# Kernel optimization log

Measured on AMD Instinct MI355X. Metric: run time of the kernel, lower is better.

The kernel has to match this reference:

```python
import jax, jax.numpy as jnp
import numpy as np
from jax import lax

H, W, K, MAXN = 93, 44, 2, 24          # face grid, hop count, (2K+1)^2-1 neighbors
HID, LAT, OUT, B = 128, 1024, 2, 8


def _neighbor_lookup():
    """Static k-hop box neighbor indices/counts for each grid position."""
    HW = H * W
    idx = np.zeros((HW, MAXN), np.int32)
    cnt = np.zeros((HW,), np.int32)
    for r in range(H):
        for c in range(W):
            p = r * W + c
            n = []
            for dr in range(-K, K + 1):
                for dc in range(-K, K + 1):
                    if dr == 0 and dc == 0:
                        continue
                    rr, cc = r + dr, c + dc
                    if 0 <= rr < H and 0 <= cc < W:
                        n.append(rr * W + cc)
            cnt[p] = len(n)
            idx[p, :len(n)] = n
    return jnp.asarray(idx), jnp.asarray(cnt)


def _gelu(x):
    return jax.nn.gelu(x, approximate=False)  # torch default GELU is exact erf


def _group_norm(x, gamma, beta, groups=8, eps=1e-5):
    b, c, h, w = x.shape
    xg = x.reshape(b, groups, c // groups, h, w)
    mu = xg.mean(axis=(2, 3, 4), keepdims=True)
    var = xg.var(axis=(2, 3, 4), keepdims=True)
    xg = (xg - mu) * lax.rsqrt(var + eps)
    return xg.reshape(b, c, h, w) * gamma[None, :, None, None] + beta[None, :, None, None]


def setup_inputs() -> dict:
    key = jax.random.key(0)
    ks = jax.random.split(key, 10)
    s = 0.05
    nbr_idx, nbr_cnt = _neighbor_lookup()
    return {
        "face_tensor": jax.random.normal(ks[0], (B, 2, H, W), jnp.float32),
        "latent_token": jax.random.normal(ks[1], (B, LAT), jnp.float32),
        "mask_2d": jax.random.randint(ks[2], (B, H, W), 0, 2, jnp.int32),
        "nbr_indices": nbr_idx,
        "nbr_counts": nbr_cnt,
        # latent_proj
        "Wl": jax.random.normal(ks[3], (LAT, HID), jnp.float32) * s,
        "bl": jnp.zeros((HID,), jnp.float32),
        # global_decoder: ConvTranspose2d(3x3,pad1) -> GN(8) -> GELU -> Conv2d(3x3,pad1) -> GELU
        "Wt": jax.random.normal(ks[4], (3, 3, HID, HID), jnp.float32) * s,
        "bt": jnp.zeros((HID,), jnp.float32),
        "g1": jnp.ones((HID,), jnp.float32),
        "b1g": jnp.zeros((HID,), jnp.float32),
        "Wc": jax.random.normal(ks[5], (3, 3, HID, HID), jnp.float32) * s,
        "bc": jnp.zeros((HID,), jnp.float32),
        # attention scorer
        "Wa": jax.random.normal(ks[6], (HID,), jnp.float32) * s,
        "ba": jnp.zeros((), jnp.float32),
        # masked_pred_head MLP
        "W1": jax.random.normal(ks[7], (2 * HID, HID), jnp.float32) * s,
        "b1": jnp.zeros((HID,), jnp.float32),
        "W2": jax.random.normal(ks[8], (HID, OUT), jnp.float32) * s,
        "b2": jnp.zeros((OUT,), jnp.float32),
    }


def reference(face_tensor, latent_token, mask_2d, nbr_indices, nbr_counts,
              Wl, bl, Wt, bt, g1, b1g, Wc, bc, Wa, ba, W1, b1, W2, b2):
    Bn, C, Hh, Ww = face_tensor.shape
    HW = Hh * Ww
    dn = ("NCHW", "HWIO", "NCHW")

    # --- feature extraction (global decoder branch) ---
    latent_cond = _gelu(latent_token @ Wl + bl)                      # (B, HID)
    x = jnp.broadcast_to(latent_cond[:, :, None, None], (Bn, HID, Hh, Ww))
    f = lax.conv_transpose(x, Wt, (1, 1), "SAME", dimension_numbers=dn) + bt[None, :, None, None]
    f = _gelu(_group_norm(f, g1, b1g))
    f = lax.conv_general_dilated(f, Wc, (1, 1), "SAME", dimension_numbers=dn) + bc[None, :, None, None]
    f = _gelu(f)
    feats = f.reshape(Bn, HID, HW).transpose(0, 2, 1)                # (B, HW, HID)

    # --- masked-neighbor attention pooling (computed for every position, padded layout) ---
    mask_flat = mask_2d.reshape(Bn, HW)
    in_range = jnp.arange(MAXN)[None, :] < nbr_counts[:, None]        # (HW, 24)
    nbr_masked = jnp.take(mask_flat, nbr_indices, axis=1)             # (B, HW, 24)
    valid = in_range[None] & (nbr_masked == 0)
    nbr_feat = jnp.take(feats, nbr_indices, axis=1)                   # (B, HW, 24, HID)
    logits = jnp.einsum("bpnh,h->bpn", nbr_feat, Wa) + ba
    logits = jnp.where(valid, logits, jnp.float32(-10000.0))
    attn = jax.nn.softmax(logits, axis=-1)
    attended = jnp.einsum("bpn,bpnh->bph", attn, nbr_feat)            # (B, HW, HID)

    combined = jnp.concatenate(
        [attended, jnp.broadcast_to(latent_cond[:, None, :], (Bn, HW, HID))], axis=-1)
    preds = _gelu(combined @ W1 + b1) @ W2 + b2                       # (B, HW, OUT)

    # --- pack masked positions to front of each row (fixed capacity HW instead of dynamic max_masked) ---
    m = mask_flat > 0
    within = jnp.cumsum(m, axis=1) - 1                                # slot for each masked position
    tgt = jnp.where(m, within, HW)                                    # unmasked go to dump slot HW
    brow = jnp.arange(Bn)[:, None]
    pred_packed = jnp.zeros((Bn, HW + 1, OUT), preds.dtype).at[brow, tgt].set(preds)[:, :HW]
    pos = jnp.arange(HW)
    rc = jnp.stack([pos // Ww, pos % Ww], axis=-1).astype(jnp.int32)  # (HW, 2)
    mask_indices = jnp.zeros((Bn, HW + 1, 2), jnp.int32).at[brow, tgt].set(
        jnp.broadcast_to(rc[None], (Bn, HW, 2)))[:, :HW]
    valid_mask = jnp.zeros((Bn, HW + 1), bool).at[brow, tgt].set(m)[:, :HW]
    return pred_packed, mask_indices, valid_mask
```

## Files before the change

### kernel.cpp

```cpp
#include <hip/hip_runtime.h>
#include <cmath>

#define HH   93
#define WWID 44
#define HWSZ 4092
#define NMAX 24
#define HID  128
#define LATD 1024
#define NB   8

__device__ __forceinline__ float gelu_f(float x) {
  return 0.5f * x * (1.0f + erff(x * 0.70710678118654752440f));
}

__device__ __constant__ int c_map[5][3] = {{-1,0,1},{0,1,1},{1,1,1},{1,1,2},{1,2,-1}};

__global__ __launch_bounds__(1024) void k_tap10(
    const float* __restrict__ latent, const float* __restrict__ Wl,
    const float* __restrict__ bl,
    const float* __restrict__ Wt, const float* __restrict__ W1, const float* __restrict__ b1p,
    float* __restrict__ u, float* __restrict__ cbo, float* __restrict__ outz)
{
  const int tap = blockIdx.x, b = blockIdx.y, tid = threadIdx.x;
  const int h4 = tid & 31, ig = tid >> 5;
  __shared__ float red[32 * HID];
  __shared__ float lc_s[HID];

  {
    const int gtid = (b * 10 + tap) * 1024 + tid;
    float4* oz = (float4*)outz;
    if (gtid < (NB*HWSZ*5)/4) oz[gtid] = make_float4(0.f, 0.f, 0.f, 0.f);
  }

  {
    const float* lat = latent + b * LATD;
    const float4* w4 = (const float4*)Wl;
    float4 a = make_float4(0.f, 0.f, 0.f, 0.f);
    for (int i0 = 0; i0 < 32; i0 += 8) {
      float  lv[8];
      float4 wv[8];
      #pragma unroll
      for (int j = 0; j < 8; ++j) {
        const int L = ig*32 + i0 + j;
        lv[j] = lat[L];
        wv[j] = w4[L*32 + h4];
      }
      #pragma unroll
      for (int j = 0; j < 8; ++j) {
        a.x = fmaf(lv[j], wv[j].x, a.x);
        a.y = fmaf(lv[j], wv[j].y, a.y);
        a.z = fmaf(lv[j], wv[j].z, a.z);
        a.w = fmaf(lv[j], wv[j].w, a.w);
      }
    }
    ((float4*)red)[ig*32 + h4] = a;
  }
  __syncthreads();
  if (tid < HID) {
    float s = bl[tid];
    #pragma unroll 8
    for (int g = 0; g < 32; ++g) s += red[g*HID + tid];
    lc_s[tid] = gelu_f(s);
  }
  __syncthreads();

  const float4* wt4 = (tap < 9) ? ((const float4*)(Wt + tap*HID*HID))
                                : ((const float4*)(W1 + HID*HID));
  float4 aa = make_float4(0.f, 0.f, 0.f, 0.f);
  #pragma unroll
  for (int j = 0; j < 4; ++j) {
    const int I = ig*4 + j;
    const float lv = lc_s[I];
    const float4 wv = wt4[I*32 + h4];
    aa.x = fmaf(lv, wv.x, aa.x); aa.y = fmaf(lv, wv.y, aa.y);
    aa.z = fmaf(lv, wv.z, aa.z); aa.w = fmaf(lv, wv.w, aa.w);
  }
  __syncthreads();
  ((float4*)red)[ig*32 + h4] = aa;
  __syncthreads();
  if (tid < HID) {
    float s = 0.f;
    #pragma unroll 8
    for (int g = 0; g < 32; ++g) s += red[g*HID + tid];
    if (tap < 9) u[(b*10 + tap)*HID + tid] = s;
    else         cbo[b*HID + tid] = b1p[tid] + s;
  }
}

__global__ __launch_bounds__(256) void k_case(
    const float* __restrict__ u, const float* __restrict__ bt,
    const float* __restrict__ g1p, const float* __restrict__ b1g,
    const float* __restrict__ Wc, const float* __restrict__ bc,
    const float* __restrict__ Wa, const float* __restrict__ ba,
    const float* __restrict__ W1,
    float* __restrict__ logito, float* __restrict__ projo)
{
  const int cs = blockIdx.x, b = blockIdx.y;
  const int r5 = cs / 5, c5 = cs % 5;
  const int tid = threadIdx.x, o4 = tid & 31, ig = tid >> 5;
  __shared__ float f2s[9 * HID];
  __shared__ float red[8 * HID];
  __shared__ float f3s[HID];
  __shared__ float red2[2];

  if (tid < HID) {
    const int t = tid;
    float uv[9];
    #pragma unroll
    for (int k = 0; k < 9; ++k) uv[k] = u[(b*10 + k)*HID + t];
    float ur[3][3];
    #pragma unroll
    for (int kc = 0; kc < 3; ++kc) {
      ur[0][kc] = uv[3+kc] + uv[6+kc];
      ur[1][kc] = uv[0+kc] + uv[3+kc] + uv[6+kc];
      ur[2][kc] = uv[0+kc] + uv[3+kc];
    }
    const float btv = bt[t];
    float f1v[9];
    #pragma unroll
    for (int a = 0; a < 3; ++a) {
      f1v[a*3+0] = btv + ur[a][1] + ur[a][2];
      f1v[a*3+1] = btv + ur[a][0] + ur[a][1] + ur[a][2];
      f1v[a*3+2] = btv + ur[a][0] + ur[a][1];
    }
    const float wr[3] = {1.f, (float)(HH-2), 1.f};
    const float wc[3] = {1.f, (float)(WWID-2), 1.f};
    float s1 = 0.f, s2 = 0.f;
    #pragma unroll
    for (int a = 0; a < 3; ++a)
      #pragma unroll
      for (int c = 0; c < 3; ++c) {
        const float w = wr[a] * wc[c];
        const float v = f1v[a*3+c];
        s1 += w * v;
        s2 += w * v * v;
      }
    #pragma unroll
    for (int off = 1; off < 16; off <<= 1) {
      s1 += __shfl_xor(s1, off);
      s2 += __shfl_xor(s2, off);
    }
    const float invN = 1.f / (float)(16 * HWSZ);
    const float mean = s1 * invN;
    const float var  = s2 * invN - mean * mean;
    const float sc = rsqrtf(var + 1e-5f) * g1p[t];
    const float sh = b1g[t] - mean * sc;
    #pragma unroll
    for (int k = 0; k < 9; ++k)
      f2s[k*HID + t] = gelu_f(fmaf(f1v[k], sc, sh));
  }
  __syncthreads();

  float4 a = make_float4(0.f, 0.f, 0.f, 0.f);
  #pragma unroll
  for (int kr = 0; kr < 3; ++kr) {
    const int rm = c_map[r5][kr];
    if (rm < 0) continue;
    #pragma unroll
    for (int kc = 0; kc < 3; ++kc) {
      const int cm = c_map[c5][kc];
      if (cm < 0) continue;
      const float4* w4 = (const float4*)(Wc + (kr*3 + kc)*HID*HID);
      const float* f2p = &f2s[(rm*3 + cm)*HID];
      #pragma unroll
      for (int i = 0; i < 16; ++i) {
        const int I = ig*16 + i;
        const float f = f2p[I];
        const float4 wv = w4[I*32 + o4];
        a.x = fmaf(f, wv.x, a.x); a.y = fmaf(f, wv.y, a.y);
        a.z = fmaf(f, wv.z, a.z); a.w = fmaf(f, wv.w, a.w);
      }
    }
  }
  ((float4*)red)[ig*32 + o4] = a;
  __syncthreads();

  if (tid < HID) {
    float s = bc[tid];
    #pragma unroll
    for (int g = 0; g < 8; ++g) s += red[g*HID + tid];
    const float f3v = gelu_f(s);
    f3s[tid] = f3v;
    float pl = f3v * Wa[tid];
    #pragma unroll
    for (int off = 1; off < 64; off <<= 1) pl += __shfl_xor(pl, off);
    if ((tid & 63) == 0) red2[tid >> 6] = pl;
  }
  __syncthreads();

  const float4* w14 = (const float4*)W1;
  float4 aa = make_float4(0.f, 0.f, 0.f, 0.f);
  #pragma unroll
  for (int i = 0; i < 16; ++i) {
    const int I = ig*16 + i;
    const float f = f3s[I];
    const float4 wv = w14[I*32 + o4];
    aa.x = fmaf(f, wv.x, aa.x); aa.y = fmaf(f, wv.y, aa.y);
    aa.z = fmaf(f, wv.z, aa.z); aa.w = fmaf(f, wv.w, aa.w);
  }
  __syncthreads();
  ((float4*)red)[ig*32 + o4] = aa;
  __syncthreads();
  if (tid < HID) {
    float s = 0.f;
    #pragma unroll
    for (int g = 0; g < 8; ++g) s += red[g*HID + tid];
    projo[(b*25 + cs)*HID + tid] = s;
  }
  if (tid == 0) logito[b*32 + cs] = red2[0] + red2[1] + ba[0];
}

__global__ __launch_bounds__(256) void k_pospack(
    const int* __restrict__ mask, const int* __restrict__ nbr_idx, const int* __restrict__ nbr_cnt,
    const float* __restrict__ logiti,
    const float* __restrict__ proji, const float* __restrict__ cbasei,
    const float* __restrict__ W2, const float* __restrict__ b2,
    float* __restrict__ out)
{
  const int b = blockIdx.y, chunk = blockIdx.x, tid = threadIdx.x;
  __shared__ float4 proj_s[25 * 32];
  __shared__ float4 cbase_s[32];
  __shared__ float  logit_s[32];
  __shared__ float  w2_s[2 * HID];
  __shared__ float  ippart[2][2];
  __shared__ int    bcnt_s[4];
  __shared__ int    wcnt_s[4];

  const float4* pj = (const float4*)(proji + b*25*HID);
  for (int i = tid; i < 25*32; i += 256) proj_s[i] = pj[i];
  if (tid < 32) cbase_s[tid] = ((const float4*)(cbasei + b*HID))[tid];
  if (tid < 32) logit_s[tid] = (tid < 25) ? logiti[b*32 + tid] : 0.f;
  w2_s[tid] = W2[tid];

  const int p0 = chunk * 128;
  {
    int cnt = 0;
    const int4* m4 = (const int4*)(mask + b*HWSZ);
    for (int i = tid; i < (p0 >> 2); i += 256) {
      const int4 v = m4[i];
      cnt += (v.x > 0) + (v.y > 0) + (v.z > 0) + (v.w > 0);
    }
    #pragma unroll
    for (int off = 1; off < 64; off <<= 1) cnt += __shfl_xor(cnt, off);
    if ((tid & 63) == 0) bcnt_s[tid >> 6] = cnt;
  }
  __syncthreads();

  if (tid < HID) {
    const float g = gelu_f(((const float*)proj_s)[12*HID + tid] + ((const float*)cbase_s)[tid]);
    float q0 = g * w2_s[tid*2 + 0];
    float q1 = g * w2_s[tid*2 + 1];
    #pragma unroll
    for (int off = 1; off < 64; off <<= 1) {
      q0 += __shfl_xor(q0, off);
      q1 += __shfl_xor(q1, off);
    }
    if ((tid & 63) == 0) { ippart[tid >> 6][0] = q0; ippart[tid >> 6][1] = q1; }
  }
  __syncthreads();
  const int   base = bcnt_s[0] + bcnt_s[1] + bcnt_s[2] + bcnt_s[3];
  const float ip0 = ippart[0][0] + ippart[1][0] + b2[0];
  const float ip1 = ippart[0][1] + ippart[1][1] + b2[1];

  const int p = p0 + (tid >> 1);
  const int half = tid & 1;
  const bool pok = (p < HWSZ);
  const int pc = pok ? p : 0;
  const int r = pc / WWID, cc = pc % WWID;
  const bool interior = (r >= 4) && (r <= HH-5) && (cc >= 4) && (cc <= WWID-5);
  const bool mp = pok && (mask[b*HWSZ + pc] > 0);

  float pr0 = ip0, pr1 = ip1;
  if (pok && !interior) {
    const int cnt = nbr_cnt[pc];
    float ev[NMAX];
    int   cid[NMAX];
    #pragma unroll
    for (int n = 0; n < NMAX; ++n) {
      const int q = nbr_idx[pc*NMAX + n];
      const int qr = q / WWID, qc = q % WWID;
      const int r5 = (qr == 0) ? 0 : (qr == 1) ? 1 : (qr == HH-2) ? 3 : (qr == HH-1) ? 4 : 2;
      const int c5 = (qc == 0) ? 0 : (qc == 1) ? 1 : (qc == WWID-2) ? 3 : (qc == WWID-1) ? 4 : 2;
      const int cd = r5*5 + c5;
      cid[n] = cd;
      const bool ok = (n < cnt) && (mask[b*HWSZ + q] == 0);
      ev[n] = ok ? logit_s[cd] : -10000.0f;
    }
    float mx = ev[0];
    #pragma unroll
    for (int n = 1; n < NMAX; ++n) mx = fmaxf(mx, ev[n]);
    float s = 0.f;
    #pragma unroll
    for (int n = 0; n < NMAX; ++n) { ev[n] = expf(ev[n] - mx); s += ev[n]; }
    const float inv = 1.f / s;

    float a0 = 0.f, a1 = 0.f;
    const int hb = half * 16;
    #pragma unroll 4
    for (int hq = 0; hq < 16; ++hq) {
      float4 a = make_float4(0.f, 0.f, 0.f, 0.f);
      #pragma unroll
      for (int n = 0; n < NMAX; ++n) {
        const float4 pv = proj_s[cid[n]*32 + hb + hq];
        const float w = ev[n];
        a.x = fmaf(w, pv.x, a.x);
        a.y = fmaf(w, pv.y, a.y);
        a.z = fmaf(w, pv.z, a.z);
        a.w = fmaf(w, pv.w, a.w);
      }
      const float4 cb = cbase_s[hb + hq];
      const int h0 = (hb + hq) * 4;
      const float g0 = gelu_f(fmaf(inv, a.x, cb.x));
      const float g1v = gelu_f(fmaf(inv, a.y, cb.y));
      const float g2 = gelu_f(fmaf(inv, a.z, cb.z));
      const float g3 = gelu_f(fmaf(inv, a.w, cb.w));
      a0 = fmaf(g0, w2_s[(h0+0)*2+0], a0); a1 = fmaf(g0, w2_s[(h0+0)*2+1], a1);
      a0 = fmaf(g1v, w2_s[(h0+1)*2+0], a0); a1 = fmaf(g1v, w2_s[(h0+1)*2+1], a1);
      a0 = fmaf(g2, w2_s[(h0+2)*2+0], a0); a1 = fmaf(g2, w2_s[(h0+2)*2+1], a1);
      a0 = fmaf(g3, w2_s[(h0+3)*2+0], a0); a1 = fmaf(g3, w2_s[(h0+3)*2+1], a1);
    }
    a0 += __shfl_xor(a0, 1);
    a1 += __shfl_xor(a1, 1);
    pr0 = a0 + b2[0];
    pr1 = a1 + b2[1];
  }

  const unsigned long long bal = __ballot(mp && half == 0);
  const int lane = tid & 63;
  const int myidx = __popcll(bal & ((1ull << lane) - 1ull));
  if (lane == 0) wcnt_s[tid >> 6] = (int)__popcll(bal);
  __syncthreads();
  int wbase = 0;
  for (int w = 0; w < (tid >> 6); ++w) wbase += wcnt_s[w];
  if (mp && half == 0) {
    const int slot = base + wbase + myidx;
    float* predo = out + b*HWSZ*2;
    float* idxo  = out + NB*HWSZ*2 + b*HWSZ*2;
    float* valo  = out + NB*HWSZ*4 + b*HWSZ;
    predo[slot*2 + 0] = pr0;
    predo[slot*2 + 1] = pr1;
    idxo[slot*2 + 0] = (float)r;
    idxo[slot*2 + 1] = (float)cc;
    valo[slot] = 1.0f;
  }
}

extern "C" void kernel_launch(void* const* d_in, const int* in_sizes, int n_in,
                              void* d_out, int out_size, void* d_ws, size_t ws_size,
                              hipStream_t stream) {
  (void)in_sizes; (void)n_in; (void)out_size; (void)ws_size;
  const float* latent  = (const float*)d_in[1];
  const int*   mask    = (const int*)d_in[2];
  const int*   nbr_idx = (const int*)d_in[3];
  const int*   nbr_cnt = (const int*)d_in[4];
  const float* Wl  = (const float*)d_in[5];
  const float* bl  = (const float*)d_in[6];
  const float* Wt  = (const float*)d_in[7];
  const float* bt  = (const float*)d_in[8];
  const float* g1p = (const float*)d_in[9];
  const float* b1g = (const float*)d_in[10];
  const float* Wc  = (const float*)d_in[11];
  const float* bc  = (const float*)d_in[12];
  const float* Wa  = (const float*)d_in[13];
  const float* ba  = (const float*)d_in[14];
  const float* W1  = (const float*)d_in[15];
  const float* b1p = (const float*)d_in[16];
  const float* W2  = (const float*)d_in[17];
  const float* b2  = (const float*)d_in[18];

  float* ws    = (float*)d_ws;
  float* u     = ws;
  float* logit = ws + 10240;
  float* proj  = ws + 10496;
  float* cbase = ws + 36096;

  dim3 gA(10, NB);
  k_tap10<<<gA, 1024, 0, stream>>>(latent, Wl, bl, Wt, W1, b1p, u, cbase, (float*)d_out);
  dim3 gB(25, NB);
  k_case<<<gB, 256, 0, stream>>>(u, bt, g1p, b1g, Wc, bc, Wa, ba, W1, logit, proj);
  dim3 gC(32, NB);
  k_pospack<<<gC, 256, 0, stream>>>(mask, nbr_idx, nbr_cnt, logit, proj, cbase, W2, b2,
                                    (float*)d_out);
}
```

Before: 47.07 us.

## Precompute per-chunk mask prefix counts in extra k_case block; pad proj_s rows

```diff
diff --git a/kernel.cpp b/kernel.cpp
--- a/kernel.cpp
+++ b/kernel.cpp
@@ -92,12 +92,34 @@
     const float* __restrict__ g1p, const float* __restrict__ b1g,
     const float* __restrict__ Wc, const float* __restrict__ bc,
     const float* __restrict__ Wa, const float* __restrict__ ba,
-    const float* __restrict__ W1,
-    float* __restrict__ logito, float* __restrict__ projo)
+    const float* __restrict__ W1, const int* __restrict__ mask,
+    float* __restrict__ logito, float* __restrict__ projo, int* __restrict__ chunkbase)
 {
   const int cs = blockIdx.x, b = blockIdx.y;
+  const int tid = threadIdx.x;
+
+  if (cs == 25) {
+    if (tid < 32) {
+      const int4* m4 = (const int4*)(mask + b*HWSZ);
+      const int n4 = (tid == 31) ? 31 : 32;
+      int cnt = 0;
+      for (int i = 0; i < n4; ++i) {
+        const int4 v = m4[tid*32 + i];
+        cnt += (v.x > 0) + (v.y > 0) + (v.z > 0) + (v.w > 0);
+      }
+      int s = cnt;
+      #pragma unroll
+      for (int off = 1; off < 32; off <<= 1) {
+        const int t = __shfl_up(s, off);
+        if (tid >= off) s += t;
+      }
+      chunkbase[b*32 + tid] = s - cnt;
+    }
+    return;
+  }
+
   const int r5 = cs / 5, c5 = cs % 5;
-  const int tid = threadIdx.x, o4 = tid & 31, ig = tid >> 5;
+  const int o4 = tid & 31, ig = tid >> 5;
   __shared__ float f2s[9 * HID];
   __shared__ float red[8 * HID];
   __shared__ float f3s[HID];
@@ -215,39 +237,26 @@
     const float* __restrict__ logiti,
     const float* __restrict__ proji, const float* __restrict__ cbasei,
     const float* __restrict__ W2, const float* __restrict__ b2,
+    const int* __restrict__ chunkbase,
     float* __restrict__ out)
 {
   const int b = blockIdx.y, chunk = blockIdx.x, tid = threadIdx.x;
-  __shared__ float4 proj_s[25 * 32];
+  __shared__ float4 proj_s[25 * 33];
   __shared__ float4 cbase_s[32];
   __shared__ float  logit_s[32];
   __shared__ float  w2_s[2 * HID];
   __shared__ float  ippart[2][2];
-  __shared__ int    bcnt_s[4];
   __shared__ int    wcnt_s[4];
 
   const float4* pj = (const float4*)(proji + b*25*HID);
-  for (int i = tid; i < 25*32; i += 256) proj_s[i] = pj[i];
+  for (int i = tid; i < 25*32; i += 256) proj_s[(i >> 5)*33 + (i & 31)] = pj[i];
   if (tid < 32) cbase_s[tid] = ((const float4*)(cbasei + b*HID))[tid];
   if (tid < 32) logit_s[tid] = (tid < 25) ? logiti[b*32 + tid] : 0.f;
   w2_s[tid] = W2[tid];
-
-  const int p0 = chunk * 128;
-  {
-    int cnt = 0;
-    const int4* m4 = (const int4*)(mask + b*HWSZ);
-    for (int i = tid; i < (p0 >> 2); i += 256) {
-      const int4 v = m4[i];
-      cnt += (v.x > 0) + (v.y > 0) + (v.z > 0) + (v.w > 0);
-    }
-    #pragma unroll
-    for (int off = 1; off < 64; off <<= 1) cnt += __shfl_xor(cnt, off);
-    if ((tid & 63) == 0) bcnt_s[tid >> 6] = cnt;
-  }
-  __syncthreads();
-
-  if (tid < HID) {
-    const float g = gelu_f(((const float*)proj_s)[12*HID + tid] + ((const float*)cbase_s)[tid]);
+  __syncthreads();
+
+  if (tid < HID) {
+    const float g = gelu_f(((const float*)proj_s)[12*33*4 + tid] + ((const float*)cbase_s)[tid]);
     float q0 = g * w2_s[tid*2 + 0];
     float q1 = g * w2_s[tid*2 + 1];
     #pragma unroll
@@ -258,10 +267,11 @@
     if ((tid & 63) == 0) { ippart[tid >> 6][0] = q0; ippart[tid >> 6][1] = q1; }
   }
   __syncthreads();
-  const int   base = bcnt_s[0] + bcnt_s[1] + bcnt_s[2] + bcnt_s[3];
+  const int   base = chunkbase[b*32 + chunk];
   const float ip0 = ippart[0][0] + ippart[1][0] + b2[0];
   const float ip1 = ippart[0][1] + ippart[1][1] + b2[1];
 
+  const int p0 = chunk * 128;
   const int p = p0 + (tid >> 1);
   const int half = tid & 1;
   const bool pok = (p < HWSZ);
@@ -301,7 +311,7 @@
       float4 a = make_float4(0.f, 0.f, 0.f, 0.f);
       #pragma unroll
       for (int n = 0; n < NMAX; ++n) {
-        const float4 pv = proj_s[cid[n]*32 + hb + hq];
+        const float4 pv = proj_s[cid[n]*33 + hb + hq];
         const float w = ev[n];
         a.x = fmaf(w, pv.x, a.x);
         a.y = fmaf(w, pv.y, a.y);
@@ -373,12 +383,14 @@
   float* logit = ws + 10240;
   float* proj  = ws + 10496;
   float* cbase = ws + 36096;
+  int*   chunkbase = (int*)(ws + 37120);
 
   dim3 gA(10, NB);
   k_tap10<<<gA, 1024, 0, stream>>>(latent, Wl, bl, Wt, W1, b1p, u, cbase, (float*)d_out);
-  dim3 gB(25, NB);
-  k_case<<<gB, 256, 0, stream>>>(u, bt, g1p, b1g, Wc, bc, Wa, ba, W1, logit, proj);
+  dim3 gB(26, NB);
+  k_case<<<gB, 256, 0, stream>>>(u, bt, g1p, b1g, Wc, bc, Wa, ba, W1, mask,
+                                 logit, proj, chunkbase);
   dim3 gC(32, NB);
   k_pospack<<<gC, 256, 0, stream>>>(mask, nbr_idx, nbr_cnt, logit, proj, cbase, W2, b2,
-                                    (float*)d_out);
-}
+                                    chunkbase, (float*)d_out);
+}
```

New measurement: 45.30 us. 1.04x faster.
